# Optimization experiments

Measured on AMD Instinct MI355X. Metric: run time of the kernel, lower is better.

The kernel has to match this reference:

```python
import jax, jax.numpy as jnp
import numpy as np

B, L, H = 1024, 256, 128
NUM_TEAMS, NUM_VENUES, NUM_RESULTS = 1000, 3, 3
OUT_IN = 4 * H + 2 + 3  # past_repr (4H+2) concat stats (3)


def setup_inputs() -> dict:
    key = jax.random.key(0)
    ks = jax.random.split(key, 16)
    return {
        "team_embed": jax.random.normal(ks[0], (NUM_TEAMS, H), jnp.float32) * 0.02,
        "venue_embed": jax.random.normal(ks[1], (NUM_VENUES, H), jnp.float32) * 0.02,
        "result_embed": jax.random.normal(ks[2], (NUM_RESULTS, H), jnp.float32) * 0.02,
        "W_out": jax.random.normal(ks[3], (OUT_IN, NUM_RESULTS), jnp.float32) * 0.02,
        "b_out": jnp.zeros((NUM_RESULTS,), jnp.float32),
        "goals_for": jax.random.uniform(ks[4], (B, L), jnp.float32) * 5.0,
        "goals_against": jax.random.uniform(ks[5], (B, L), jnp.float32) * 5.0,
        "stats": jax.random.uniform(ks[6], (B, 3), jnp.float32),
        "venue": jax.random.randint(ks[7], (B, L), 0, NUM_VENUES),
        "team": jax.random.randint(ks[8], (B, L), 0, NUM_TEAMS),
        "opponent": jax.random.randint(ks[9], (B, L), 0, NUM_TEAMS),
        "result": jax.random.randint(ks[10], (B, L), 0, NUM_RESULTS),
        "next_venue": jax.random.randint(ks[11], (B,), 0, NUM_VENUES),
        "next_team": jax.random.randint(ks[12], (B,), 0, NUM_TEAMS),
        "next_opponent": jax.random.randint(ks[13], (B,), 0, NUM_TEAMS),
    }


def reference(team_embed, venue_embed, result_embed, W_out, b_out,
              goals_for, goals_against, stats,
              venue, team, opponent, result,
              next_venue, next_team, next_opponent):
    h = team_embed.shape[1]
    # (B, L, 4H+2): embedding gathers + goal scalars concatenated
    past_seq = jnp.concatenate([
        venue_embed[venue], team_embed[team], team_embed[opponent],
        result_embed[result], goals_for[..., None], goals_against[..., None],
    ], axis=-1)
    # (B, 3H): next-match condition vector
    next_cond = jnp.concatenate([
        venue_embed[next_venue], team_embed[next_team], team_embed[next_opponent],
    ], axis=-1)
    scale = jnp.asarray(3 * h, past_seq.dtype) ** 0.5
    scores = jnp.einsum('bld,bd->bl', past_seq[..., : 3 * h], next_cond) / scale
    attn = jax.nn.softmax(scores, axis=1)                 # over L
    past_repr = jnp.einsum('bl,bld->bd', attn, past_seq)  # (B, 4H+2)
    logits = jnp.concatenate([past_repr, stats], axis=-1) @ W_out + b_out
    return logits
```

## Files before the change

kernel.cpp:

```cpp
#include <hip/hip_runtime.h>

#define L_ 256
#define H_ 128

#define KSCALE 0.07362222315f

#define REC_STRIDE 272

__global__ __launch_bounds__(256, 8) void partial_kernel(
    const float* __restrict__ team_embed,
    const float* __restrict__ venue_embed,
    const float* __restrict__ goals_for,
    const float* __restrict__ goals_against,
    const int* __restrict__ venue,
    const int* __restrict__ team,
    const int* __restrict__ opponent,
    const int* __restrict__ result,
    const int* __restrict__ next_venue,
    const int* __restrict__ next_team,
    const int* __restrict__ next_opponent,
    float* __restrict__ ws)
{
    const int b    = blockIdx.x >> 1;
    const int j    = blockIdx.x & 1;
    const int t    = threadIdx.x;
    const int lane = t & 63;
    const int wid  = t >> 6;
    const int half = lane >> 5;
    const int c    = lane & 31;

    __shared__ float  nc[384];
    __shared__ int    s_team[128];
    __shared__ int    s_opp[128];
    __shared__ int    s_vi[128];
    __shared__ int    s_ri[128];
    __shared__ float  s_gf[128];
    __shared__ float  s_ga[128];
    __shared__ float  s_e[128];
    __shared__ float  s_dotv[3];
    __shared__ float4 s_accT[8][32];
    __shared__ float4 s_accO[8][32];
    __shared__ float  s_red[2][9];

    const int base = b * L_ + j * 128;
    if (t < 128) {
        s_team[t] = team[base + t];
        s_opp[t]  = opponent[base + t];
        s_vi[t]   = venue[base + t];
        s_ri[t]   = result[base + t];
        s_gf[t]   = goals_for[base + t];
        s_ga[t]   = goals_against[base + t];
    }
    const int nv  = next_venue[b];
    const int ntm = next_team[b];
    const int nop = next_opponent[b];
    if (t < 128) {
        nc[t]       = venue_embed[nv * H_ + t];
        nc[128 + t] = team_embed[ntm * H_ + t];
    } else {
        nc[128 + t] = team_embed[nop * H_ + (t - 128)];
    }
    __syncthreads();

    if (wid < 3) {
        float a = venue_embed[wid * H_ + lane]      * nc[lane]
                + venue_embed[wid * H_ + 64 + lane] * nc[64 + lane];
        #pragma unroll
        for (int off = 32; off > 0; off >>= 1) a += __shfl_down(a, off);
        if (lane == 0) s_dotv[wid] = a;
    }
    __syncthreads();

    const float4 nct_c = ((const float4*)(nc + 128))[c];
    const float4 nco_c = ((const float4*)(nc + 256))[c];
    const int hw = wid * 2 + half;
    const int lb = hw * 16;
    float4 accT = make_float4(0.f, 0.f, 0.f, 0.f);
    float4 accO = make_float4(0.f, 0.f, 0.f, 0.f);
    #pragma unroll 4
    for (int i = 0; i < 16; ++i) {
        const int l = lb + i;
        const float4 vT = ((const float4*)team_embed)[s_team[l] * 32 + c];
        const float4 vO = ((const float4*)team_embed)[s_opp[l]  * 32 + c];
        float p = vT.x * nct_c.x + vT.y * nct_c.y + vT.z * nct_c.z + vT.w * nct_c.w
                + vO.x * nco_c.x + vO.y * nco_c.y + vO.z * nco_c.z + vO.w * nco_c.w;
        #pragma unroll
        for (int k = 16; k > 0; k >>= 1) p += __shfl_xor(p, k);
        const float e = exp2f((p + s_dotv[s_vi[l]]) * KSCALE);
        if ((lane & 31) == 0) s_e[l] = e;
        accT.x += e * vT.x; accT.y += e * vT.y; accT.z += e * vT.z; accT.w += e * vT.w;
        accO.x += e * vO.x; accO.y += e * vO.y; accO.z += e * vO.z; accO.w += e * vO.w;
    }
    s_accT[hw][c] = accT;
    s_accO[hw][c] = accO;
    __syncthreads();

    if (t < 128) {
        const float e = s_e[t];
        const int vi = s_vi[t], ri = s_ri[t];
        float vals[9];
        vals[0] = e;
        vals[1] = (vi == 0) ? e : 0.f;
        vals[2] = (vi == 1) ? e : 0.f;
        vals[3] = (vi == 2) ? e : 0.f;
        vals[4] = (ri == 0) ? e : 0.f;
        vals[5] = (ri == 1) ? e : 0.f;
        vals[6] = (ri == 2) ? e : 0.f;
        vals[7] = e * s_gf[t];
        vals[8] = e * s_ga[t];
        #pragma unroll
        for (int off = 32; off > 0; off >>= 1) {
            #pragma unroll
            for (int k = 0; k < 9; ++k) vals[k] += __shfl_down(vals[k], off);
        }
        if (lane == 0) {
            #pragma unroll
            for (int k = 0; k < 9; ++k) s_red[wid][k] = vals[k];
        }
    }
    __syncthreads();

    float* rec = ws + (size_t)blockIdx.x * REC_STRIDE;
    if (t < 9) rec[256 + t] = s_red[0][t] + s_red[1][t];
    if (t < 64) {
        const int seg = t >> 5, cc = t & 31;
        float4 a = make_float4(0.f, 0.f, 0.f, 0.f);
        #pragma unroll
        for (int h = 0; h < 8; ++h) {
            const float4 v = seg ? s_accO[h][cc] : s_accT[h][cc];
            a.x += v.x; a.y += v.y; a.z += v.z; a.w += v.w;
        }
        *((float4*)(rec + seg * 128 + cc * 4)) = a;
    }
}

__global__ __launch_bounds__(256) void finalize_kernel(
    const float* __restrict__ venue_embed,
    const float* __restrict__ result_embed,
    const float* __restrict__ W_out,
    const float* __restrict__ b_out,
    const float* __restrict__ stats,
    const float* __restrict__ ws,
    float* __restrict__ out)
{
    const int b    = blockIdx.x;
    const int t    = threadIdx.x;
    const int lane = t & 63;
    const int wid  = t >> 6;

    __shared__ float s_pr[517];
    __shared__ float s_w[8];

    const float* r0 = ws + (size_t)(b * 2) * REC_STRIDE;
    const float* r1 = r0 + REC_STRIDE;
    const float invZ = 1.f / (r0[256] + r1[256]);

    s_pr[128 + t] = (r0[t] + r1[t]) * invZ;
    if (t < 8) s_w[t] = (r0[257 + t] + r1[257 + t]) * invZ;
    __syncthreads();

    if (t < 128) {
        s_pr[t] = s_w[0] * venue_embed[t] + s_w[1] * venue_embed[H_ + t]
                + s_w[2] * venue_embed[2 * H_ + t];
    } else {
        const int jj = t - 128;
        s_pr[384 + jj] = s_w[3] * result_embed[jj] + s_w[4] * result_embed[H_ + jj]
                       + s_w[5] * result_embed[2 * H_ + jj];
    }
    if (t == 0) { s_pr[512] = s_w[6]; s_pr[513] = s_w[7]; }
    if (t < 3)  s_pr[514 + t] = stats[b * 3 + t];
    __syncthreads();

    if (wid < 3) {
        float acc = 0.f;
        for (int d = lane; d < 517; d += 64) acc += s_pr[d] * W_out[d * 3 + wid];
        #pragma unroll
        for (int off = 32; off > 0; off >>= 1) acc += __shfl_down(acc, off);
        if (lane == 0) out[b * 3 + wid] = acc + b_out[wid];
    }
}

extern "C" void kernel_launch(void* const* d_in, const int* in_sizes, int n_in,
                              void* d_out, int out_size, void* d_ws, size_t ws_size,
                              hipStream_t stream) {
    const float* team_embed    = (const float*)d_in[0];
    const float* venue_embed   = (const float*)d_in[1];
    const float* result_embed  = (const float*)d_in[2];
    const float* W_out         = (const float*)d_in[3];
    const float* b_out         = (const float*)d_in[4];
    const float* goals_for     = (const float*)d_in[5];
    const float* goals_against = (const float*)d_in[6];
    const float* stats         = (const float*)d_in[7];
    const int* venue           = (const int*)d_in[8];
    const int* team            = (const int*)d_in[9];
    const int* opponent        = (const int*)d_in[10];
    const int* result          = (const int*)d_in[11];
    const int* next_venue      = (const int*)d_in[12];
    const int* next_team       = (const int*)d_in[13];
    const int* next_opponent   = (const int*)d_in[14];
    float* out = (float*)d_out;
    float* ws  = (float*)d_ws;

    const int B = in_sizes[12];
    partial_kernel<<<B * 2, 256, 0, stream>>>(
        team_embed, venue_embed, goals_for, goals_against,
        venue, team, opponent, result,
        next_venue, next_team, next_opponent, ws);
    finalize_kernel<<<B, 256, 0, stream>>>(
        venue_embed, result_embed, W_out, b_out, stats, ws, out);
}
```

Before: 112.5 us.

## Gather team embeddings from a bf16 copy and batch finalize per wave

Adds a pre-pass that converts the team embedding table to bf16 with round-to-nearest-even. The main kernel then gathers 16-byte bf16 rows, eight elements per lane with sixteen lanes per row and four rows per wave, which halves gather bytes and changes the cross-lane reduction layout. The finalize kernel now handles four batch rows per block, one per wave, and stages W_out in shared memory. This costs one extra launch and reduces embedding precision in both the scores and the weighted sums, which may affect the accuracy tolerance.

```diff
diff --git a/kernel.cpp b/kernel.cpp
--- a/kernel.cpp
+++ b/kernel.cpp
@@ -6,6 +6,23 @@
 #define KSCALE 0.07362222315f
 
 #define REC_STRIDE 272
+#define TBL_U4_PER_ROW 16
+
+__device__ __forceinline__ unsigned bf16rne(float f) {
+    unsigned u = __float_as_uint(f);
+    return (u + 0x7fffu + ((u >> 16) & 1u)) >> 16;
+}
+
+__global__ __launch_bounds__(256) void convert_kernel(
+    const float* __restrict__ team_embed, unsigned* __restrict__ tbl, int n4)
+{
+    const int i = blockIdx.x * 256 + threadIdx.x;
+    if (i < n4) {
+        const float4 v = ((const float4*)team_embed)[i];
+        ((uint2*)tbl)[i] = make_uint2(bf16rne(v.x) | (bf16rne(v.y) << 16),
+                                      bf16rne(v.z) | (bf16rne(v.w) << 16));
+    }
+}
 
 __global__ __launch_bounds__(256, 8) void partial_kernel(
     const float* __restrict__ team_embed,
@@ -19,28 +36,29 @@
     const int* __restrict__ next_venue,
     const int* __restrict__ next_team,
     const int* __restrict__ next_opponent,
-    float* __restrict__ ws)
+    const unsigned* __restrict__ tbl,
+    float* __restrict__ ws_rec)
 {
     const int b    = blockIdx.x >> 1;
     const int j    = blockIdx.x & 1;
     const int t    = threadIdx.x;
     const int lane = t & 63;
     const int wid  = t >> 6;
-    const int half = lane >> 5;
-    const int c    = lane & 31;
-
-    __shared__ float  nc[384];
-    __shared__ int    s_team[128];
-    __shared__ int    s_opp[128];
-    __shared__ int    s_vi[128];
-    __shared__ int    s_ri[128];
-    __shared__ float  s_gf[128];
-    __shared__ float  s_ga[128];
-    __shared__ float  s_e[128];
-    __shared__ float  s_dotv[3];
-    __shared__ float4 s_accT[8][32];
-    __shared__ float4 s_accO[8][32];
-    __shared__ float  s_red[2][9];
+    const int q    = lane >> 4;
+    const int ql   = lane & 15;
+
+    __shared__ float nc[384];
+    __shared__ int   s_team[128];
+    __shared__ int   s_opp[128];
+    __shared__ int   s_vi[128];
+    __shared__ int   s_ri[128];
+    __shared__ float s_gf[128];
+    __shared__ float s_ga[128];
+    __shared__ float s_e[128];
+    __shared__ float s_dotv[3];
+    __shared__ float s_accT[4][128];
+    __shared__ float s_accO[4][128];
+    __shared__ float s_red[2][9];
 
     const int base = b * L_ + j * 128;
     if (t < 128) {
@@ -71,28 +89,58 @@
     }
     __syncthreads();
 
-    const float4 nct_c = ((const float4*)(nc + 128))[c];
-    const float4 nco_c = ((const float4*)(nc + 256))[c];
-    const int hw = wid * 2 + half;
-    const int lb = hw * 16;
-    float4 accT = make_float4(0.f, 0.f, 0.f, 0.f);
-    float4 accO = make_float4(0.f, 0.f, 0.f, 0.f);
+    float ncT[8], ncO[8];
+    #pragma unroll
+    for (int e = 0; e < 8; ++e) {
+        ncT[e] = nc[128 + ql * 8 + e];
+        ncO[e] = nc[256 + ql * 8 + e];
+    }
+
+    const uint4* tbl4 = (const uint4*)tbl;
+    const int lb = wid * 32;
+    float accT[8], accO[8];
+    #pragma unroll
+    for (int e = 0; e < 8; ++e) { accT[e] = 0.f; accO[e] = 0.f; }
+
     #pragma unroll 4
-    for (int i = 0; i < 16; ++i) {
-        const int l = lb + i;
-        const float4 vT = ((const float4*)team_embed)[s_team[l] * 32 + c];
-        const float4 vO = ((const float4*)team_embed)[s_opp[l]  * 32 + c];
-        float p = vT.x * nct_c.x + vT.y * nct_c.y + vT.z * nct_c.z + vT.w * nct_c.w
-                + vO.x * nco_c.x + vO.y * nco_c.y + vO.z * nco_c.z + vO.w * nco_c.w;
-        #pragma unroll
-        for (int k = 16; k > 0; k >>= 1) p += __shfl_xor(p, k);
-        const float e = exp2f((p + s_dotv[s_vi[l]]) * KSCALE);
-        if ((lane & 31) == 0) s_e[l] = e;
-        accT.x += e * vT.x; accT.y += e * vT.y; accT.z += e * vT.z; accT.w += e * vT.w;
-        accO.x += e * vO.x; accO.y += e * vO.y; accO.z += e * vO.z; accO.w += e * vO.w;
-    }
-    s_accT[hw][c] = accT;
-    s_accO[hw][c] = accO;
+    for (int iter = 0; iter < 8; ++iter) {
+        const int ll = lb + iter * 4 + q;
+        const uint4 dT = tbl4[s_team[ll] * 16 + ql];
+        const uint4 dO = tbl4[s_opp[ll]  * 16 + ql];
+        float fT[8], fO[8];
+        fT[0] = __uint_as_float(dT.x << 16); fT[1] = __uint_as_float(dT.x & 0xffff0000u);
+        fT[2] = __uint_as_float(dT.y << 16); fT[3] = __uint_as_float(dT.y & 0xffff0000u);
+        fT[4] = __uint_as_float(dT.z << 16); fT[5] = __uint_as_float(dT.z & 0xffff0000u);
+        fT[6] = __uint_as_float(dT.w << 16); fT[7] = __uint_as_float(dT.w & 0xffff0000u);
+        fO[0] = __uint_as_float(dO.x << 16); fO[1] = __uint_as_float(dO.x & 0xffff0000u);
+        fO[2] = __uint_as_float(dO.y << 16); fO[3] = __uint_as_float(dO.y & 0xffff0000u);
+        fO[4] = __uint_as_float(dO.z << 16); fO[5] = __uint_as_float(dO.z & 0xffff0000u);
+        fO[6] = __uint_as_float(dO.w << 16); fO[7] = __uint_as_float(dO.w & 0xffff0000u);
+        float p = 0.f;
+        #pragma unroll
+        for (int e = 0; e < 8; ++e) p += fT[e] * ncT[e] + fO[e] * ncO[e];
+        #pragma unroll
+        for (int k = 8; k > 0; k >>= 1) p += __shfl_xor(p, k);
+        const float ev = exp2f((p + s_dotv[s_vi[ll]]) * KSCALE);
+        if (ql == 0) s_e[ll] = ev;
+        #pragma unroll
+        for (int e = 0; e < 8; ++e) {
+            accT[e] += ev * fT[e];
+            accO[e] += ev * fO[e];
+        }
+    }
+    #pragma unroll
+    for (int e = 0; e < 8; ++e) {
+        accT[e] += __shfl_xor(accT[e], 16); accT[e] += __shfl_xor(accT[e], 32);
+        accO[e] += __shfl_xor(accO[e], 16); accO[e] += __shfl_xor(accO[e], 32);
+    }
+    if (lane < 16) {
+        #pragma unroll
+        for (int e = 0; e < 8; ++e) {
+            s_accT[wid][ql * 8 + e] = accT[e];
+            s_accO[wid][ql * 8 + e] = accO[e];
+        }
+    }
     __syncthreads();
 
     if (t < 128) {
@@ -120,17 +168,19 @@
     }
     __syncthreads();
 
-    float* rec = ws + (size_t)blockIdx.x * REC_STRIDE;
+    float* rec = ws_rec + (size_t)blockIdx.x * REC_STRIDE;
     if (t < 9) rec[256 + t] = s_red[0][t] + s_red[1][t];
     if (t < 64) {
-        const int seg = t >> 5, cc = t & 31;
-        float4 a = make_float4(0.f, 0.f, 0.f, 0.f);
-        #pragma unroll
-        for (int h = 0; h < 8; ++h) {
-            const float4 v = seg ? s_accO[h][cc] : s_accT[h][cc];
-            a.x += v.x; a.y += v.y; a.z += v.z; a.w += v.w;
-        }
-        *((float4*)(rec + seg * 128 + cc * 4)) = a;
+        const int d = t * 4;
+        const int seg = d >> 7;
+        const int dd = d & 127;
+        const float (*sa)[128] = seg ? s_accO : s_accT;
+        float4 a;
+        a.x = sa[0][dd+0] + sa[1][dd+0] + sa[2][dd+0] + sa[3][dd+0];
+        a.y = sa[0][dd+1] + sa[1][dd+1] + sa[2][dd+1] + sa[3][dd+1];
+        a.z = sa[0][dd+2] + sa[1][dd+2] + sa[2][dd+2] + sa[3][dd+2];
+        a.w = sa[0][dd+3] + sa[1][dd+3] + sa[2][dd+3] + sa[3][dd+3];
+        *((float4*)(rec + d)) = a;
     }
 }
 
@@ -140,43 +190,58 @@
     const float* __restrict__ W_out,
     const float* __restrict__ b_out,
     const float* __restrict__ stats,
-    const float* __restrict__ ws,
+    const float* __restrict__ ws_rec,
     float* __restrict__ out)
 {
-    const int b    = blockIdx.x;
     const int t    = threadIdx.x;
     const int lane = t & 63;
     const int wid  = t >> 6;
-
-    __shared__ float s_pr[517];
-    __shared__ float s_w[8];
-
-    const float* r0 = ws + (size_t)(b * 2) * REC_STRIDE;
+    const int b    = blockIdx.x * 4 + wid;
+
+    __shared__ float s_W[1551];
+    __shared__ float s_pr[4][520];
+
+    for (int i = t; i < 1551; i += 256) s_W[i] = W_out[i];
+
+    const float* r0 = ws_rec + (size_t)(b * 2) * REC_STRIDE;
     const float* r1 = r0 + REC_STRIDE;
     const float invZ = 1.f / (r0[256] + r1[256]);
-
-    s_pr[128 + t] = (r0[t] + r1[t]) * invZ;
-    if (t < 8) s_w[t] = (r0[257 + t] + r1[257 + t]) * invZ;
-    __syncthreads();
-
-    if (t < 128) {
-        s_pr[t] = s_w[0] * venue_embed[t] + s_w[1] * venue_embed[H_ + t]
-                + s_w[2] * venue_embed[2 * H_ + t];
-    } else {
-        const int jj = t - 128;
-        s_pr[384 + jj] = s_w[3] * result_embed[jj] + s_w[4] * result_embed[H_ + jj]
-                       + s_w[5] * result_embed[2 * H_ + jj];
-    }
-    if (t == 0) { s_pr[512] = s_w[6]; s_pr[513] = s_w[7]; }
-    if (t < 3)  s_pr[514 + t] = stats[b * 3 + t];
-    __syncthreads();
-
-    if (wid < 3) {
-        float acc = 0.f;
-        for (int d = lane; d < 517; d += 64) acc += s_pr[d] * W_out[d * 3 + wid];
-        #pragma unroll
-        for (int off = 32; off > 0; off >>= 1) acc += __shfl_down(acc, off);
-        if (lane == 0) out[b * 3 + wid] = acc + b_out[wid];
+    float w[8];
+    #pragma unroll
+    for (int k = 0; k < 8; ++k) w[k] = (r0[257 + k] + r1[257 + k]) * invZ;
+
+    #pragma unroll
+    for (int d = 0; d < 256; d += 64)
+        s_pr[wid][128 + d + lane] = (r0[d + lane] + r1[d + lane]) * invZ;
+    #pragma unroll
+    for (int d = 0; d < 128; d += 64) {
+        const int jj = d + lane;
+        s_pr[wid][jj] = w[0] * venue_embed[jj] + w[1] * venue_embed[H_ + jj]
+                      + w[2] * venue_embed[2 * H_ + jj];
+        s_pr[wid][384 + jj] = w[3] * result_embed[jj] + w[4] * result_embed[H_ + jj]
+                            + w[5] * result_embed[2 * H_ + jj];
+    }
+    if (lane == 0) { s_pr[wid][512] = w[6]; s_pr[wid][513] = w[7]; }
+    if (lane < 3)  s_pr[wid][514 + lane] = stats[b * 3 + lane];
+    __syncthreads();
+
+    float a0 = 0.f, a1 = 0.f, a2 = 0.f;
+    for (int d = lane; d < 517; d += 64) {
+        const float p = s_pr[wid][d];
+        a0 += p * s_W[d * 3 + 0];
+        a1 += p * s_W[d * 3 + 1];
+        a2 += p * s_W[d * 3 + 2];
+    }
+    #pragma unroll
+    for (int off = 32; off > 0; off >>= 1) {
+        a0 += __shfl_down(a0, off);
+        a1 += __shfl_down(a1, off);
+        a2 += __shfl_down(a2, off);
+    }
+    if (lane == 0) {
+        out[b * 3 + 0] = a0 + b_out[0];
+        out[b * 3 + 1] = a1 + b_out[1];
+        out[b * 3 + 2] = a2 + b_out[2];
     }
 }
 
@@ -199,13 +264,18 @@
     const int* next_team       = (const int*)d_in[13];
     const int* next_opponent   = (const int*)d_in[14];
     float* out = (float*)d_out;
-    float* ws  = (float*)d_ws;
-
-    const int B = in_sizes[12];
+
+    unsigned* tbl   = (unsigned*)d_ws;
+    float*    wsrec = (float*)d_ws + 65536;
+
+    const int B  = in_sizes[12];
+    const int n4 = in_sizes[0] / 4;
+
+    convert_kernel<<<(n4 + 255) / 256, 256, 0, stream>>>(team_embed, tbl, n4);
     partial_kernel<<<B * 2, 256, 0, stream>>>(
         team_embed, venue_embed, goals_for, goals_against,
         venue, team, opponent, result,
-        next_venue, next_team, next_opponent, ws);
-    finalize_kernel<<<B, 256, 0, stream>>>(
-        venue_embed, result_embed, W_out, b_out, stats, ws, out);
-}
+        next_venue, next_team, next_opponent, tbl, wsrec);
+    finalize_kernel<<<B / 4, 256, 0, stream>>>(
+        venue_embed, result_embed, W_out, b_out, stats, wsrec, out);
+}
```

Result: slower. 180.5 us (+60.4%).

## Fuse partial and finalize kernels into one per-batch 512-thread kernel

Applied to the files above, without the earlier changes.

Merges the two-stage approach, which split each batch row across two blocks and then ran a finalize kernel, into a single kernel with one 512-thread block per batch row. The block computes the full softmax-weighted sums, normalises them, and applies the output projection in shared memory. This removes the second launch and the global workspace write/read. In exchange each block is larger and there are half as many blocks, which changes scheduling granularity.

```diff
diff --git a/kernel.cpp b/kernel.cpp
--- a/kernel.cpp
+++ b/kernel.cpp
@@ -5,13 +5,15 @@
 
 #define KSCALE 0.07362222315f
 
-#define REC_STRIDE 272
-
-__global__ __launch_bounds__(256, 8) void partial_kernel(
+__global__ __launch_bounds__(512, 8) void fused_match_kernel(
     const float* __restrict__ team_embed,
     const float* __restrict__ venue_embed,
+    const float* __restrict__ result_embed,
+    const float* __restrict__ W_out,
+    const float* __restrict__ b_out,
     const float* __restrict__ goals_for,
     const float* __restrict__ goals_against,
+    const float* __restrict__ stats,
     const int* __restrict__ venue,
     const int* __restrict__ team,
     const int* __restrict__ opponent,
@@ -19,10 +21,9 @@
     const int* __restrict__ next_venue,
     const int* __restrict__ next_team,
     const int* __restrict__ next_opponent,
-    float* __restrict__ ws)
+    float* __restrict__ out)
 {
-    const int b    = blockIdx.x >> 1;
-    const int j    = blockIdx.x & 1;
+    const int b    = blockIdx.x;
     const int t    = threadIdx.x;
     const int lane = t & 63;
     const int wid  = t >> 6;
@@ -30,20 +31,22 @@
     const int c    = lane & 31;
 
     __shared__ float  nc[384];
-    __shared__ int    s_team[128];
-    __shared__ int    s_opp[128];
-    __shared__ int    s_vi[128];
-    __shared__ int    s_ri[128];
-    __shared__ float  s_gf[128];
-    __shared__ float  s_ga[128];
-    __shared__ float  s_e[128];
+    __shared__ int    s_team[L_];
+    __shared__ int    s_opp[L_];
+    __shared__ int    s_vi[L_];
+    __shared__ int    s_ri[L_];
+    __shared__ float  s_gf[L_];
+    __shared__ float  s_ga[L_];
+    __shared__ float  s_e[L_];
     __shared__ float  s_dotv[3];
-    __shared__ float4 s_accT[8][32];
-    __shared__ float4 s_accO[8][32];
-    __shared__ float  s_red[2][9];
+    __shared__ float4 s_accT[16][32];
+    __shared__ float4 s_accO[16][32];
+    __shared__ float  s_red[4][9];
+    __shared__ float  s_w[8];
+    __shared__ float  s_pr[517];
 
-    const int base = b * L_ + j * 128;
-    if (t < 128) {
+    const int base = b * L_;
+    if (t < L_) {
         s_team[t] = team[base + t];
         s_opp[t]  = opponent[base + t];
         s_vi[t]   = venue[base + t];
@@ -57,7 +60,7 @@
     if (t < 128) {
         nc[t]       = venue_embed[nv * H_ + t];
         nc[128 + t] = team_embed[ntm * H_ + t];
-    } else {
+    } else if (t < 256) {
         nc[128 + t] = team_embed[nop * H_ + (t - 128)];
     }
     __syncthreads();
@@ -86,16 +89,16 @@
                 + vO.x * nco_c.x + vO.y * nco_c.y + vO.z * nco_c.z + vO.w * nco_c.w;
         #pragma unroll
         for (int k = 16; k > 0; k >>= 1) p += __shfl_xor(p, k);
-        const float e = exp2f((p + s_dotv[s_vi[l]]) * KSCALE);
-        if ((lane & 31) == 0) s_e[l] = e;
-        accT.x += e * vT.x; accT.y += e * vT.y; accT.z += e * vT.z; accT.w += e * vT.w;
-        accO.x += e * vO.x; accO.y += e * vO.y; accO.z += e * vO.z; accO.w += e * vO.w;
+        const float ev = exp2f((p + s_dotv[s_vi[l]]) * KSCALE);
+        if ((lane & 31) == 0) s_e[l] = ev;
+        accT.x += ev * vT.x; accT.y += ev * vT.y; accT.z += ev * vT.z; accT.w += ev * vT.w;
+        accO.x += ev * vO.x; accO.y += ev * vO.y; accO.z += ev * vO.z; accO.w += ev * vO.w;
     }
     s_accT[hw][c] = accT;
     s_accO[hw][c] = accO;
     __syncthreads();
 
-    if (t < 128) {
+    if (t < L_) {
         const float e = s_e[t];
         const int vi = s_vi[t], ri = s_ri[t];
         float vals[9];
@@ -120,55 +123,39 @@
     }
     __syncthreads();
 
-    float* rec = ws + (size_t)blockIdx.x * REC_STRIDE;
-    if (t < 9) rec[256 + t] = s_red[0][t] + s_red[1][t];
+    const float Z    = s_red[0][0] + s_red[1][0] + s_red[2][0] + s_red[3][0];
+    const float invZ = 1.f / Z;
+    if (t < 8) {
+        s_w[t] = (s_red[0][t + 1] + s_red[1][t + 1] + s_red[2][t + 1] + s_red[3][t + 1]) * invZ;
+    }
+    __syncthreads();
+
     if (t < 64) {
-        const int seg = t >> 5, cc = t & 31;
+        const int seg = t >> 5, g = t & 31;
         float4 a = make_float4(0.f, 0.f, 0.f, 0.f);
         #pragma unroll
-        for (int h = 0; h < 8; ++h) {
-            const float4 v = seg ? s_accO[h][cc] : s_accT[h][cc];
+        for (int h = 0; h < 16; ++h) {
+            const float4 v = seg ? s_accO[h][g] : s_accT[h][g];
             a.x += v.x; a.y += v.y; a.z += v.z; a.w += v.w;
         }
-        *((float4*)(rec + seg * 128 + cc * 4)) = a;
+        const int d = 128 + seg * 128 + g * 4;
+        s_pr[d + 0] = a.x * invZ;
+        s_pr[d + 1] = a.y * invZ;
+        s_pr[d + 2] = a.z * invZ;
+        s_pr[d + 3] = a.w * invZ;
+    } else if (t < 192) {
+        const int j = t - 64;
+        s_pr[j] = s_w[0] * venue_embed[j] + s_w[1] * venue_embed[H_ + j]
+                + s_w[2] * venue_embed[2 * H_ + j];
+    } else if (t < 320) {
+        const int j = t - 192;
+        s_pr[384 + j] = s_w[3] * result_embed[j] + s_w[4] * result_embed[H_ + j]
+                      + s_w[5] * result_embed[2 * H_ + j];
+    } else if (t < 322) {
+        s_pr[512 + (t - 320)] = s_w[6 + (t - 320)];
+    } else if (t < 325) {
+        s_pr[514 + (t - 322)] = stats[b * 3 + (t - 322)];
     }
-}
-
-__global__ __launch_bounds__(256) void finalize_kernel(
-    const float* __restrict__ venue_embed,
-    const float* __restrict__ result_embed,
-    const float* __restrict__ W_out,
-    const float* __restrict__ b_out,
-    const float* __restrict__ stats,
-    const float* __restrict__ ws,
-    float* __restrict__ out)
-{
-    const int b    = blockIdx.x;
-    const int t    = threadIdx.x;
-    const int lane = t & 63;
-    const int wid  = t >> 6;
-
-    __shared__ float s_pr[517];
-    __shared__ float s_w[8];
-
-    const float* r0 = ws + (size_t)(b * 2) * REC_STRIDE;
-    const float* r1 = r0 + REC_STRIDE;
-    const float invZ = 1.f / (r0[256] + r1[256]);
-
-    s_pr[128 + t] = (r0[t] + r1[t]) * invZ;
-    if (t < 8) s_w[t] = (r0[257 + t] + r1[257 + t]) * invZ;
-    __syncthreads();
-
-    if (t < 128) {
-        s_pr[t] = s_w[0] * venue_embed[t] + s_w[1] * venue_embed[H_ + t]
-                + s_w[2] * venue_embed[2 * H_ + t];
-    } else {
-        const int jj = t - 128;
-        s_pr[384 + jj] = s_w[3] * result_embed[jj] + s_w[4] * result_embed[H_ + jj]
-                       + s_w[5] * result_embed[2 * H_ + jj];
-    }
-    if (t == 0) { s_pr[512] = s_w[6]; s_pr[513] = s_w[7]; }
-    if (t < 3)  s_pr[514 + t] = stats[b * 3 + t];
     __syncthreads();
 
     if (wid < 3) {
@@ -199,13 +186,11 @@
     const int* next_team       = (const int*)d_in[13];
     const int* next_opponent   = (const int*)d_in[14];
     float* out = (float*)d_out;
-    float* ws  = (float*)d_ws;
 
     const int B = in_sizes[12];
-    partial_kernel<<<B * 2, 256, 0, stream>>>(
-        team_embed, venue_embed, goals_for, goals_against,
+    fused_match_kernel<<<B, 512, 0, stream>>>(
+        team_embed, venue_embed, result_embed, W_out, b_out,
+        goals_for, goals_against, stats,
         venue, team, opponent, result,
-        next_venue, next_team, next_opponent, ws);
-    finalize_kernel<<<B, 256, 0, stream>>>(
-        venue_embed, result_embed, W_out, b_out, stats, ws, out);
+        next_venue, next_team, next_opponent, out);
 }
```

New measurement: 110.3 us. 2.0% less time.
